# Performance work log

Measured on AMD Instinct MI355X. Metric: run time of the kernel, lower is better.

## Reference

```python
import jax, jax.numpy as jnp
import numpy as np

A, B, S, AD, H, NH = 8, 32768, 128, 16, 64, 4
D = H // NH  # attend_dim = 16
MAX_ACTION = 1.0


def setup_inputs() -> dict:
    key = jax.random.key(0)
    ks = jax.random.split(key, 16)
    sc = 0.05
    return {
        'states': jax.random.normal(ks[0], (A, B, S), jnp.float32),
        'actions': jax.random.normal(ks[1], (A, B, AD), jnp.float32),
        'Ws': jax.random.normal(ks[2], (S, H), jnp.float32) * sc,
        'bs': jnp.zeros((H,), jnp.float32),
        'We': jax.random.normal(ks[3], (S + AD, H), jnp.float32) * sc,
        'be': jnp.zeros((H,), jnp.float32),
        'Wk': jax.random.normal(ks[4], (NH, H, D), jnp.float32) * sc,
        'Wsel': jax.random.normal(ks[5], (NH, H, D), jnp.float32) * sc,
        'Wv': jax.random.normal(ks[6], (NH, H, D), jnp.float32) * sc,
        'bv': jnp.zeros((NH, D), jnp.float32),
        'W1': jax.random.normal(ks[7], (2 * H, H), jnp.float32) * sc,
        'b1': jnp.zeros((H,), jnp.float32),
        'W2': jax.random.normal(ks[8], (H, 1), jnp.float32) * sc,
        'b2': jnp.zeros((1,), jnp.float32),
    }


def reference(states, actions, Ws, bs, We, be, Wk, Wsel, Wv, bv, W1, b1, W2, b2):
    # per-agent encoders (shared params, as in the torch module)
    s_enc = jax.nn.relu(jnp.einsum('abs,sh->abh', states, Ws) + bs)          # [A,B,H]
    sa = jnp.concatenate([states, actions / MAX_ACTION], axis=-1)            # [A,B,S+AD]
    sa_enc = jax.nn.relu(jnp.einsum('abi,ih->abh', sa, We) + be)             # [A,B,H]

    # per-head keys / values / selectors (n = head axis)
    keys = jnp.einsum('abh,nhd->nabd', sa_enc, Wk)                           # [NH,A,B,D]
    vals = jax.nn.relu(jnp.einsum('abh,nhd->nabd', sa_enc, Wv) + bv[:, None, None, :])
    sel = jnp.einsum('abh,nhd->nabd', s_enc, Wsel)                           # [NH,A,B,D]

    # exclude-self attention over agents == masked softmax over agent axis j
    logits = jnp.einsum('nibd,njbd->nibj', sel, keys) / jnp.sqrt(jnp.float32(D))
    self_mask = jnp.eye(A, dtype=bool)                                       # [A(i),A(j)]
    logits = jnp.where(self_mask[None, :, None, :], -1e9, logits)
    w = jax.nn.softmax(logits, axis=-1)                                      # [NH,A,B,A]
    other = jnp.einsum('nibj,njbd->nibd', w, vals)                           # [NH,A,B,D]
    other_cat = jnp.transpose(other, (1, 2, 0, 3)).reshape(A, B, NH * D)     # [A,B,H]

    critic_in = jnp.concatenate([sa_enc, other_cat], axis=-1)                # [A,B,2H]
    h = jax.nn.relu(jnp.einsum('abi,ih->abh', critic_in, W1) + b1)
    q = jnp.einsum('abh,ho->abo', h, W2) + b2                                # [A,B,1]
    return q
```

## Files before the change

### kernel.cpp

```cpp
#include <hip/hip_runtime.h>
#include <hip/hip_bf16.h>

#define A_N 8
#define B_N 32768
#define S_N 128
#define AD_N 16

typedef __attribute__((ext_vector_type(8))) short short8;
typedef __attribute__((ext_vector_type(4))) float floatx4;
typedef __attribute__((ext_vector_type(4))) int intx4;

#define MFMA16(a, b, c) __builtin_amdgcn_mfma_f32_16x16x32_bf16(a, b, c, 0, 0, 0)
#define SBAR() __builtin_amdgcn_sched_barrier(0)

__device__ __forceinline__ short f2bf(float f) {
    __hip_bfloat16 h = __float2bfloat16(f);
    return *reinterpret_cast<short*>(&h);
}
__device__ __forceinline__ int pk(float a, float b) {
    __hip_bfloat162 p = __float22bfloat162_rn(make_float2(a, b));
    return *reinterpret_cast<int*>(&p);
}
__device__ __forceinline__ short8 mk8(int a, int b, int c, int d) {
    intx4 v = {a, b, c, d};
    return *reinterpret_cast<short8*>(&v);
}
__device__ __forceinline__ void pk2(short8& r, int i, float a, float b) {
    __hip_bfloat162 p = __float22bfloat162_rn(make_float2(a, b));
    short2 s = *reinterpret_cast<short2*>(&p);
    r[i] = s.x; r[i + 1] = s.y;
}
__device__ __forceinline__ short8 cvt8(float4 x0, float4 x1) {
    short8 r;
    pk2(r, 0, x0.x, x0.y); pk2(r, 2, x0.z, x0.w);
    pk2(r, 4, x1.x, x1.y); pk2(r, 6, x1.z, x1.w);
    return r;
}

__device__ __forceinline__ int chperm(int p) {
    return 32 * (p >> 5) + 16 * ((p & 7) >> 2) + 4 * ((p >> 3) & 3) + (p & 3);
}

#define OFF_Ws   10240
#define OFF_Wk   18432
#define OFF_Wsel 22528
#define OFF_Wv   26624
#define OFF_W1   30720
#define W_TOTAL  38912

__global__ void prep_weights(const float* __restrict__ Ws, const float* __restrict__ We,
                             const float* __restrict__ be,
                             const float* __restrict__ Wk, const float* __restrict__ Wsel,
                             const float* __restrict__ Wv, const float* __restrict__ W1,
                             short* __restrict__ w) {
    int idx = blockIdx.x * 256 + threadIdx.x;
    if (idx >= W_TOTAL) return;
    float v = 0.f;
    int i, base;
    if (idx < OFF_Ws)        { i = idx;            base = 0; }
    else if (idx < OFF_Wk)   { i = idx - OFF_Ws;   base = 1; }
    else if (idx < OFF_Wsel) { i = idx - OFF_Wk;   base = 2; }
    else if (idx < OFF_Wv)   { i = idx - OFF_Wsel; base = 3; }
    else if (idx < OFF_W1)   { i = idx - OFF_Wv;   base = 4; }
    else                     { i = idx - OFF_W1;   base = 5; }
    const int e   = i & 7;
    const int f   = i >> 3;
    const int ch  = f & 63;
    const int slq = f >> 6;
    const int p   = (slq >> 2) * 32 + (slq & 3) * 8 + e;
    if (base == 0)      v = (p < 144) ? We[p * 64 + ch] : (p == 144 ? be[ch] : 0.f);
    else if (base == 1) v = Ws[p * 64 + ch];
    else if (base == 2) v = Wk[(ch >> 4) * 1024 + chperm(p) * 16 + (ch & 15)];
    else if (base == 3) v = Wsel[(ch >> 4) * 1024 + chperm(p) * 16 + (ch & 15)];
    else if (base == 4) v = Wv[(ch >> 4) * 1024 + chperm(p) * 16 + (ch & 15)];
    else                v = W1[chperm(p) * 64 + ch];
    w[idx] = f2bf(v);
}

#define PAIRS 4

__global__ __launch_bounds__(512, 2)
void attention_critic_mfma(
    const float* __restrict__ states, const float* __restrict__ actions,
    const float* __restrict__ bs, const float* __restrict__ bv,
    const float* __restrict__ b1, const float* __restrict__ W2,
    const float* __restrict__ b2,
    const short* __restrict__ wts, float* __restrict__ out)
{
    __shared__ __align__(16) short smem[W_TOTAL];

    const int tid  = threadIdx.x;
    const int wv   = tid >> 6;
    const int lane = tid & 63;
    const int lq   = lane >> 4;
    const int ln   = lane & 15;

    for (int c = wv; c < 76; c += 8) {
        const unsigned int* g = reinterpret_cast<const unsigned int*>(wts + c * 512) + lane * 4;
        __builtin_amdgcn_global_load_lds(g, reinterpret_cast<unsigned int*>(smem + c * 512), 16, 0, 0);
    }

    const int lo = lq * 512 + ln * 8;
    const short* lbA = smem + lo;
    const short* lbB = smem + OFF_Wv + lo;

    float bS4[4], bv4[4], b14[4], w24[4];
    #pragma unroll
    for (int nt = 0; nt < 4; ++nt) {
        bS4[nt] = bs[nt * 16 + ln];
        bv4[nt] = bv[nt * 16 + ln];
        b14[nt] = b1[nt * 16 + ln];
        w24[nt] = W2[nt * 16 + ln];
    }
    const float b2v = b2[0];

    const int bbase = blockIdx.x * (PAIRS * 32);
    const int aA  = ln & 7;
    const int blA = ln >> 3;
    const float* srow = states  + ((long)aA * B_N + bbase + wv * 2 + blA) * S_N;
    const float* arow = actions + ((long)aA * B_N + bbase + wv * 2 + blA) * AD_N;

    __syncthreads();

    const floatx4 z = {0.f, 0.f, 0.f, 0.f};

    #pragma unroll 1
    for (int t = 0; t < PAIRS; ++t) {
        const int b0 = bbase + t * 32;

        short8 xf0[5], xf1[5];
        #pragma unroll
        for (int s = 0; s < 4; ++s) {
            float4 a0 = *reinterpret_cast<const float4*>(srow + s * 32 + lq * 8);
            float4 a1 = *reinterpret_cast<const float4*>(srow + s * 32 + lq * 8 + 4);
            float4 c0 = *reinterpret_cast<const float4*>(srow + 16 * S_N + s * 32 + lq * 8);
            float4 c1 = *reinterpret_cast<const float4*>(srow + 16 * S_N + s * 32 + lq * 8 + 4);
            xf0[s] = cvt8(a0, a1);
            xf1[s] = cvt8(c0, c1);
        }
        {
            short8 t0 = {0, 0, 0, 0, 0, 0, 0, 0}, t1 = t0;
            if (lq < 2) {
                float4 a0 = *reinterpret_cast<const float4*>(arow + lq * 8);
                float4 a1 = *reinterpret_cast<const float4*>(arow + lq * 8 + 4);
                float4 c0 = *reinterpret_cast<const float4*>(arow + 16 * AD_N + lq * 8);
                float4 c1 = *reinterpret_cast<const float4*>(arow + 16 * AD_N + lq * 8 + 4);
                t0 = cvt8(a0, a1);
                t1 = cvt8(c0, c1);
            } else if (lq == 2) {
                t0[0] = (short)0x3F80;
                t1[0] = (short)0x3F80;
            }
            xf0[4] = t0; xf1[4] = t1;
        }
        srow += 32 * S_N; arow += 32 * AD_N;

        short8 fE0[2], fE1[2];
        {
            floatx4 acc0[4] = {z, z, z, z}, acc1[4] = {z, z, z, z};
            #pragma unroll
            for (int s = 0; s < 5; ++s)
                #pragma unroll
                for (int nt = 0; nt < 4; ++nt) {
                    short8 wf = *reinterpret_cast<const short8*>(lbA + s * 2048 + nt * 128);
                    acc0[nt] = MFMA16(wf, xf0[s], acc0[nt]);
                    acc1[nt] = MFMA16(wf, xf1[s], acc1[nt]);
                }
            int p0[4][2], p1[4][2];
            #pragma unroll
            for (int nt = 0; nt < 4; ++nt) {
                p0[nt][0] = pk(fmaxf(acc0[nt][0], 0.f), fmaxf(acc0[nt][1], 0.f));
                p0[nt][1] = pk(fmaxf(acc0[nt][2], 0.f), fmaxf(acc0[nt][3], 0.f));
                p1[nt][0] = pk(fmaxf(acc1[nt][0], 0.f), fmaxf(acc1[nt][1], 0.f));
                p1[nt][1] = pk(fmaxf(acc1[nt][2], 0.f), fmaxf(acc1[nt][3], 0.f));
            }
            fE0[0] = mk8(p0[0][0], p0[0][1], p0[1][0], p0[1][1]);
            fE0[1] = mk8(p0[2][0], p0[2][1], p0[3][0], p0[3][1]);
            fE1[0] = mk8(p1[0][0], p1[0][1], p1[1][0], p1[1][1]);
            fE1[1] = mk8(p1[2][0], p1[2][1], p1[3][0], p1[3][1]);
        }
        SBAR();

        short8 fS0[2], fS1[2];
        {
            floatx4 acc0[4] = {z, z, z, z}, acc1[4] = {z, z, z, z};
            #pragma unroll
            for (int s = 0; s < 4; ++s)
                #pragma unroll
                for (int nt = 0; nt < 4; ++nt) {
                    short8 wf = *reinterpret_cast<const short8*>(lbA + OFF_Ws + s * 2048 + nt * 128);
                    acc0[nt] = MFMA16(wf, xf0[s], acc0[nt]);
                    acc1[nt] = MFMA16(wf, xf1[s], acc1[nt]);
                }
            int p0[4][2], p1[4][2];
            #pragma unroll
            for (int nt = 0; nt < 4; ++nt) {
                p0[nt][0] = pk(fmaxf(acc0[nt][0] + bS4[nt], 0.f), fmaxf(acc0[nt][1] + bS4[nt], 0.f));
                p0[nt][1] = pk(fmaxf(acc0[nt][2] + bS4[nt], 0.f), fmaxf(acc0[nt][3] + bS4[nt], 0.f));
                p1[nt][0] = pk(fmaxf(acc1[nt][0] + bS4[nt], 0.f), fmaxf(acc1[nt][1] + bS4[nt], 0.f));
                p1[nt][1] = pk(fmaxf(acc1[nt][2] + bS4[nt], 0.f), fmaxf(acc1[nt][3] + bS4[nt], 0.f));
            }
            fS0[0] = mk8(p0[0][0], p0[0][1], p0[1][0], p0[1][1]);
            fS0[1] = mk8(p0[2][0], p0[2][1], p0[3][0], p0[3][1]);
            fS1[0] = mk8(p1[0][0], p1[0][1], p1[1][0], p1[1][1]);
            fS1[1] = mk8(p1[2][0], p1[2][1], p1[3][0], p1[3][1]);
        }
        SBAR();

        int kp0[4][2], sp0[4][2], kp1[4][2], sp1[4][2];
        {
            floatx4 aK0[4] = {z, z, z, z}, aS0[4] = {z, z, z, z};
            floatx4 aK1[4] = {z, z, z, z}, aS1[4] = {z, z, z, z};
            #pragma unroll
            for (int s = 0; s < 2; ++s)
                #pragma unroll
                for (int nt = 0; nt < 4; ++nt) {
                    short8 wk = *reinterpret_cast<const short8*>(lbA + OFF_Wk   + s * 2048 + nt * 128);
                    short8 ws = *reinterpret_cast<const short8*>(lbA + OFF_Wsel + s * 2048 + nt * 128);
                    aK0[nt] = MFMA16(wk, fE0[s], aK0[nt]);
                    aK1[nt] = MFMA16(wk, fE1[s], aK1[nt]);
                    aS0[nt] = MFMA16(ws, fS0[s], aS0[nt]);
                    aS1[nt] = MFMA16(ws, fS1[s], aS1[nt]);
                }
            #pragma unroll
            for (int nt = 0; nt < 4; ++nt) {
                kp0[nt][0] = pk(aK0[nt][0], aK0[nt][1]); kp0[nt][1] = pk(aK0[nt][2], aK0[nt][3]);
                sp0[nt][0] = pk(aS0[nt][0], aS0[nt][1]); sp0[nt][1] = pk(aS0[nt][2], aS0[nt][3]);
                kp1[nt][0] = pk(aK1[nt][0], aK1[nt][1]); kp1[nt][1] = pk(aK1[nt][2], aK1[nt][3]);
                sp1[nt][0] = pk(aS1[nt][0], aS1[nt][1]); sp1[nt][1] = pk(aS1[nt][2], aS1[nt][3]);
            }
        }
        SBAR();

        int pV0[4][2], pV1[4][2];
        {
            floatx4 a0[4] = {z, z, z, z}, a1[4] = {z, z, z, z};
            #pragma unroll
            for (int s = 0; s < 2; ++s)
                #pragma unroll
                for (int nt = 0; nt < 4; ++nt) {
                    short8 wf = *reinterpret_cast<const short8*>(lbB + s * 2048 + nt * 128);
                    a0[nt] = MFMA16(fE0[s], wf, a0[nt]);
                    a1[nt] = MFMA16(fE1[s], wf, a1[nt]);
                }
            #pragma unroll
            for (int nt = 0; nt < 4; ++nt) {
                pV0[nt][0] = pk(fmaxf(a0[nt][0] + bv4[nt], 0.f), fmaxf(a0[nt][1] + bv4[nt], 0.f));
                pV0[nt][1] = pk(fmaxf(a0[nt][2] + bv4[nt], 0.f), fmaxf(a0[nt][3] + bv4[nt], 0.f));
                pV1[nt][0] = pk(fmaxf(a1[nt][0] + bv4[nt], 0.f), fmaxf(a1[nt][1] + bv4[nt], 0.f));
                pV1[nt][1] = pk(fmaxf(a1[nt][2] + bv4[nt], 0.f), fmaxf(a1[nt][3] + bv4[nt], 0.f));
            }
        }
        SBAR();

        int pO0[4][2], pO1[4][2];
        {
            const bool sameb = ((lq >> 1) == (ln >> 3));
            #pragma unroll
            for (int tt = 0; tt < 2; ++tt) {
                int (*kp)[2] = tt ? kp1 : kp0;
                int (*sp)[2] = tt ? sp1 : sp0;
                int (*pV)[2] = tt ? pV1 : pV0;
                int (*pO)[2] = tt ? pO1 : pO0;
                #pragma unroll
                for (int nt = 0; nt < 4; ++nt) {
                    short8 fa = mk8(kp[nt][0], kp[nt][1], 0, 0);
                    short8 fb = mk8(sp[nt][0], sp[nt][1], 0, 0);
                    floatx4 L = MFMA16(fa, fb, z);
                    float lg[4];
                    #pragma unroll
                    for (int i = 0; i < 4; ++i) {
                        const bool valid = sameb && (4 * lq + i != ln);
                        lg[i] = valid ? L[i] * 0.25f : -1e9f;
                    }
                    float m = fmaxf(fmaxf(lg[0], lg[1]), fmaxf(lg[2], lg[3]));
                    m = fmaxf(m, __shfl_xor(m, 16, 64));
                    m = fmaxf(m, __shfl_xor(m, 32, 64));
                    float e0 = __expf(lg[0] - m), e1 = __expf(lg[1] - m);
                    float e2 = __expf(lg[2] - m), e3 = __expf(lg[3] - m);
                    float ss = e0 + e1 + e2 + e3;
                    ss += __shfl_xor(ss, 16, 64);
                    ss += __shfl_xor(ss, 32, 64);
                    const float inv = 1.f / ss;
                    short8 fp = mk8(pk(e0 * inv, e1 * inv), pk(e2 * inv, e3 * inv), 0, 0);
                    short8 fv = mk8(pV[nt][0], pV[nt][1], 0, 0);
                    floatx4 O = MFMA16(fv, fp, z);
                    pO[nt][0] = pk(O[0], O[1]);
                    pO[nt][1] = pk(O[2], O[3]);
                }
            }
        }
        SBAR();

        {
            short8 fO0[2] = { mk8(pO0[0][0], pO0[0][1], pO0[1][0], pO0[1][1]),
                              mk8(pO0[2][0], pO0[2][1], pO0[3][0], pO0[3][1]) };
            short8 fO1[2] = { mk8(pO1[0][0], pO1[0][1], pO1[1][0], pO1[1][1]),
                              mk8(pO1[2][0], pO1[2][1], pO1[3][0], pO1[3][1]) };
            floatx4 aH0[4] = {z, z, z, z}, aH1[4] = {z, z, z, z};
            #pragma unroll
            for (int s = 0; s < 4; ++s) {
                const short8 a0 = (s < 2) ? fE0[s] : fO0[s - 2];
                const short8 a1 = (s < 2) ? fE1[s] : fO1[s - 2];
                #pragma unroll
                for (int nt = 0; nt < 4; ++nt) {
                    short8 w1 = *reinterpret_cast<const short8*>(lbB + 4096 + s * 2048 + nt * 128);
                    aH0[nt] = MFMA16(a0, w1, aH0[nt]);
                    aH1[nt] = MFMA16(a1, w1, aH1[nt]);
                }
            }
            #pragma unroll
            for (int tt = 0; tt < 2; ++tt) {
                floatx4* aH = tt ? aH1 : aH0;
                float p0 = 0.f, p1 = 0.f, p2 = 0.f, p3 = 0.f;
                #pragma unroll
                for (int nt = 0; nt < 4; ++nt) {
                    p0 += fmaxf(aH[nt][0] + b14[nt], 0.f) * w24[nt];
                    p1 += fmaxf(aH[nt][1] + b14[nt], 0.f) * w24[nt];
                    p2 += fmaxf(aH[nt][2] + b14[nt], 0.f) * w24[nt];
                    p3 += fmaxf(aH[nt][3] + b14[nt], 0.f) * w24[nt];
                }
                #pragma unroll
                for (int mk = 1; mk < 16; mk <<= 1) {
                    p0 += __shfl_xor(p0, mk, 64);
                    p1 += __shfl_xor(p1, mk, 64);
                    p2 += __shfl_xor(p2, mk, 64);
                    p3 += __shfl_xor(p3, mk, 64);
                }
                if (ln == 0) {
                    float pr[4] = {p0, p1, p2, p3};
                    const int bt = b0 + tt * 16;
                    #pragma unroll
                    for (int i = 0; i < 4; ++i) {
                        const int slot = lq * 4 + i;
                        out[(long)(slot & 7) * B_N + bt + wv * 2 + (slot >> 3)] = pr[i] + b2v;
                    }
                }
            }
        }
        SBAR();
    }
}

extern "C" void kernel_launch(void* const* d_in, const int* in_sizes, int n_in,
                              void* d_out, int out_size, void* d_ws, size_t ws_size,
                              hipStream_t stream) {
    const float* states  = (const float*)d_in[0];
    const float* actions = (const float*)d_in[1];
    const float* Ws      = (const float*)d_in[2];
    const float* bs      = (const float*)d_in[3];
    const float* We      = (const float*)d_in[4];
    const float* be      = (const float*)d_in[5];
    const float* Wk      = (const float*)d_in[6];
    const float* Wsel    = (const float*)d_in[7];
    const float* Wv      = (const float*)d_in[8];
    const float* bv      = (const float*)d_in[9];
    const float* W1      = (const float*)d_in[10];
    const float* b1      = (const float*)d_in[11];
    const float* W2      = (const float*)d_in[12];
    const float* b2      = (const float*)d_in[13];
    short* wts = (short*)d_ws;
    float* out = (float*)d_out;

    prep_weights<<<(W_TOTAL + 255) / 256, 256, 0, stream>>>(Ws, We, be, Wk, Wsel, Wv, W1, wts);
    attention_critic_mfma<<<B_N / (PAIRS * 32), 512, 0, stream>>>(
        states, actions, bs, bv, b1, W2, b2, wts, out);
}
```

Baseline: 234.9 us.

## Stage states/actions tiles into LDS asynchronously with swizzle and prefetch

Replaces direct per-thread global float4 loads of states and actions with global_load_lds staging into a per-wave swizzled LDS buffer. The next half-tile is prefetched while the current one runs its encoder MFMAs, so global latency is hidden behind compute. Phase-1 encoding is split into two sequential half-tile passes instead of interleaved dual accumulators. The cost is about 74KB of extra LDS per block and explicit waitcnt barriers, which may reduce occupancy (2 blocks of 512 threads) and cut MFMA interleaving.

Result: no change. 238.0 us (+1.3%).

```diff
diff --git a/kernel.cpp b/kernel.cpp
--- a/kernel.cpp
+++ b/kernel.cpp
@@ -35,6 +35,12 @@
     pk2(r, 0, x0.x, x0.y); pk2(r, 2, x0.z, x0.w);
     pk2(r, 4, x1.x, x1.y); pk2(r, 6, x1.z, x1.w);
     return r;
+}
+__device__ __forceinline__ void wait_lgkm() {
+    asm volatile("s_waitcnt lgkmcnt(0)" ::: "memory");
+}
+__device__ __forceinline__ void wait_vm() {
+    asm volatile("s_waitcnt vmcnt(0)" ::: "memory");
 }
 
 __device__ __forceinline__ int chperm(int p) {
@@ -79,6 +85,94 @@
 
 #define PAIRS 4
 
+#define XB_WAVE 9216
+
+__device__ __forceinline__ void stage_tile(const float* __restrict__ states,
+                                           const float* __restrict__ actions,
+                                           char* xb, int btw, int lane) {
+    const int bl  = lane >> 5;
+    const int c16 = (lane & 31) << 4;
+    #pragma unroll
+    for (int a = 0; a < 8; ++a) {
+        const int r = 2 * a + bl;
+        const char* src = (const char*)states
+            + (((long)(a * B_N + btw + bl)) << 9)
+            + (c16 ^ ((r & 7) << 4));
+        __builtin_amdgcn_global_load_lds((const unsigned int*)src,
+            (unsigned int*)(xb + a * 1024), 16, 0, 0);
+    }
+    {
+        const int ra  = lane >> 2;
+        const char* src = (const char*)actions
+            + (((long)((lane >> 3) * B_N + btw + ((lane >> 2) & 1))) << 6)
+            + (((lane & 3) << 4) ^ ((ra & 6) << 3));
+        __builtin_amdgcn_global_load_lds((const unsigned int*)src,
+            (unsigned int*)(xb + 8192), 16, 0, 0);
+    }
+}
+
+__device__ __forceinline__ void load_xf(const char* xb, int r, int lq, short8* xf) {
+    const int ss = (r & 7) << 4;
+    const char* rb = xb + (r << 9);
+    #pragma unroll
+    for (int s = 0; s < 4; ++s) {
+        const int c = (s << 7) + (lq << 5);
+        float4 f0 = *reinterpret_cast<const float4*>(rb + ((c)      ^ ss));
+        float4 f1 = *reinterpret_cast<const float4*>(rb + ((c + 16) ^ ss));
+        xf[s] = cvt8(f0, f1);
+    }
+    short8 xt = {0, 0, 0, 0, 0, 0, 0, 0};
+    if (lq < 2) {
+        const int as = (r & 6) << 3;
+        const char* ab = xb + 8192 + (r << 6);
+        const int c = lq << 5;
+        float4 f0 = *reinterpret_cast<const float4*>(ab + ((c)      ^ as));
+        float4 f1 = *reinterpret_cast<const float4*>(ab + ((c + 16) ^ as));
+        xt = cvt8(f0, f1);
+    } else if (lq == 2) {
+        xt[0] = (short)0x3F80;
+    }
+    xf[4] = xt;
+}
+
+__device__ __forceinline__ void do_phase1(const short8* xf, const short* lbA,
+                                          const float* bS4, short8* fE, short8* fS) {
+    const floatx4 z = {0.f, 0.f, 0.f, 0.f};
+    {
+        floatx4 acc[4] = {z, z, z, z};
+        #pragma unroll
+        for (int s = 0; s < 5; ++s)
+            #pragma unroll
+            for (int nt = 0; nt < 4; ++nt)
+                acc[nt] = MFMA16(*reinterpret_cast<const short8*>(lbA + s * 2048 + nt * 128), xf[s], acc[nt]);
+        int p[4][2];
+        #pragma unroll
+        for (int nt = 0; nt < 4; ++nt) {
+            p[nt][0] = pk(fmaxf(acc[nt][0], 0.f), fmaxf(acc[nt][1], 0.f));
+            p[nt][1] = pk(fmaxf(acc[nt][2], 0.f), fmaxf(acc[nt][3], 0.f));
+        }
+        fE[0] = mk8(p[0][0], p[0][1], p[1][0], p[1][1]);
+        fE[1] = mk8(p[2][0], p[2][1], p[3][0], p[3][1]);
+    }
+    SBAR();
+    {
+        floatx4 acc[4] = {z, z, z, z};
+        #pragma unroll
+        for (int s = 0; s < 4; ++s)
+            #pragma unroll
+            for (int nt = 0; nt < 4; ++nt)
+                acc[nt] = MFMA16(*reinterpret_cast<const short8*>(lbA + OFF_Ws + s * 2048 + nt * 128), xf[s], acc[nt]);
+        int p[4][2];
+        #pragma unroll
+        for (int nt = 0; nt < 4; ++nt) {
+            p[nt][0] = pk(fmaxf(acc[nt][0] + bS4[nt], 0.f), fmaxf(acc[nt][1] + bS4[nt], 0.f));
+            p[nt][1] = pk(fmaxf(acc[nt][2] + bS4[nt], 0.f), fmaxf(acc[nt][3] + bS4[nt], 0.f));
+        }
+        fS[0] = mk8(p[0][0], p[0][1], p[1][0], p[1][1]);
+        fS[1] = mk8(p[2][0], p[2][1], p[3][0], p[3][1]);
+    }
+}
+
 __global__ __launch_bounds__(512, 2)
 void attention_critic_mfma(
     const float* __restrict__ states, const float* __restrict__ actions,
@@ -87,7 +181,7 @@
     const float* __restrict__ b2,
     const short* __restrict__ wts, float* __restrict__ out)
 {
-    __shared__ __align__(16) short smem[W_TOTAL];
+    __shared__ __align__(16) short smem[W_TOTAL + 8 * (XB_WAVE / 2)];
 
     const int tid  = threadIdx.x;
     const int wv   = tid >> 6;
@@ -103,6 +197,8 @@
     const int lo = lq * 512 + ln * 8;
     const short* lbA = smem + lo;
     const short* lbB = smem + OFF_Wv + lo;
+
+    char* xb = reinterpret_cast<char*>(smem + W_TOTAL) + wv * XB_WAVE;
 
     float bS4[4], bv4[4], b14[4], w24[4];
     #pragma unroll
@@ -115,96 +211,35 @@
     const float b2v = b2[0];
 
     const int bbase = blockIdx.x * (PAIRS * 32);
-    const int aA  = ln & 7;
-    const int blA = ln >> 3;
-    const float* srow = states  + ((long)aA * B_N + bbase + wv * 2 + blA) * S_N;
-    const float* arow = actions + ((long)aA * B_N + bbase + wv * 2 + blA) * AD_N;
-
+    const int rX = ((ln & 7) << 1) | (ln >> 3);
+
+    stage_tile(states, actions, xb, bbase + wv * 2, lane);
     __syncthreads();
 
     const floatx4 z = {0.f, 0.f, 0.f, 0.f};
 
     #pragma unroll 1
     for (int t = 0; t < PAIRS; ++t) {
-        const int b0 = bbase + t * 32;
-
-        short8 xf0[5], xf1[5];
-        #pragma unroll
-        for (int s = 0; s < 4; ++s) {
-            float4 a0 = *reinterpret_cast<const float4*>(srow + s * 32 + lq * 8);
-            float4 a1 = *reinterpret_cast<const float4*>(srow + s * 32 + lq * 8 + 4);
-            float4 c0 = *reinterpret_cast<const float4*>(srow + 16 * S_N + s * 32 + lq * 8);
-            float4 c1 = *reinterpret_cast<const float4*>(srow + 16 * S_N + s * 32 + lq * 8 + 4);
-            xf0[s] = cvt8(a0, a1);
-            xf1[s] = cvt8(c0, c1);
-        }
-        {
-            short8 t0 = {0, 0, 0, 0, 0, 0, 0, 0}, t1 = t0;
-            if (lq < 2) {
-                float4 a0 = *reinterpret_cast<const float4*>(arow + lq * 8);
-                float4 a1 = *reinterpret_cast<const float4*>(arow + lq * 8 + 4);
-                float4 c0 = *reinterpret_cast<const float4*>(arow + 16 * AD_N + lq * 8);
-                float4 c1 = *reinterpret_cast<const float4*>(arow + 16 * AD_N + lq * 8 + 4);
-                t0 = cvt8(a0, a1);
-                t1 = cvt8(c0, c1);
-            } else if (lq == 2) {
-                t0[0] = (short)0x3F80;
-                t1[0] = (short)0x3F80;
-            }
-            xf0[4] = t0; xf1[4] = t1;
-        }
-        srow += 32 * S_N; arow += 32 * AD_N;
-
-        short8 fE0[2], fE1[2];
-        {
-            floatx4 acc0[4] = {z, z, z, z}, acc1[4] = {z, z, z, z};
-            #pragma unroll
-            for (int s = 0; s < 5; ++s)
-                #pragma unroll
-                for (int nt = 0; nt < 4; ++nt) {
-                    short8 wf = *reinterpret_cast<const short8*>(lbA + s * 2048 + nt * 128);
-                    acc0[nt] = MFMA16(wf, xf0[s], acc0[nt]);
-                    acc1[nt] = MFMA16(wf, xf1[s], acc1[nt]);
-                }
-            int p0[4][2], p1[4][2];
-            #pragma unroll
-            for (int nt = 0; nt < 4; ++nt) {
-                p0[nt][0] = pk(fmaxf(acc0[nt][0], 0.f), fmaxf(acc0[nt][1], 0.f));
-                p0[nt][1] = pk(fmaxf(acc0[nt][2], 0.f), fmaxf(acc0[nt][3], 0.f));
-                p1[nt][0] = pk(fmaxf(acc1[nt][0], 0.f), fmaxf(acc1[nt][1], 0.f));
-                p1[nt][1] = pk(fmaxf(acc1[nt][2], 0.f), fmaxf(acc1[nt][3], 0.f));
-            }
-            fE0[0] = mk8(p0[0][0], p0[0][1], p0[1][0], p0[1][1]);
-            fE0[1] = mk8(p0[2][0], p0[2][1], p0[3][0], p0[3][1]);
-            fE1[0] = mk8(p1[0][0], p1[0][1], p1[1][0], p1[1][1]);
-            fE1[1] = mk8(p1[2][0], p1[2][1], p1[3][0], p1[3][1]);
-        }
-        SBAR();
-
-        short8 fS0[2], fS1[2];
-        {
-            floatx4 acc0[4] = {z, z, z, z}, acc1[4] = {z, z, z, z};
-            #pragma unroll
-            for (int s = 0; s < 4; ++s)
-                #pragma unroll
-                for (int nt = 0; nt < 4; ++nt) {
-                    short8 wf = *reinterpret_cast<const short8*>(lbA + OFF_Ws + s * 2048 + nt * 128);
-                    acc0[nt] = MFMA16(wf, xf0[s], acc0[nt]);
-                    acc1[nt] = MFMA16(wf, xf1[s], acc1[nt]);
-                }
-            int p0[4][2], p1[4][2];
-            #pragma unroll
-            for (int nt = 0; nt < 4; ++nt) {
-                p0[nt][0] = pk(fmaxf(acc0[nt][0] + bS4[nt], 0.f), fmaxf(acc0[nt][1] + bS4[nt], 0.f));
-                p0[nt][1] = pk(fmaxf(acc0[nt][2] + bS4[nt], 0.f), fmaxf(acc0[nt][3] + bS4[nt], 0.f));
-                p1[nt][0] = pk(fmaxf(acc1[nt][0] + bS4[nt], 0.f), fmaxf(acc1[nt][1] + bS4[nt], 0.f));
-                p1[nt][1] = pk(fmaxf(acc1[nt][2] + bS4[nt], 0.f), fmaxf(acc1[nt][3] + bS4[nt], 0.f));
-            }
-            fS0[0] = mk8(p0[0][0], p0[0][1], p0[1][0], p0[1][1]);
-            fS0[1] = mk8(p0[2][0], p0[2][1], p0[3][0], p0[3][1]);
-            fS1[0] = mk8(p1[0][0], p1[0][1], p1[1][0], p1[1][1]);
-            fS1[1] = mk8(p1[2][0], p1[2][1], p1[3][0], p1[3][1]);
-        }
+        const int b0   = bbase + t * 32;
+        const int btw0 = b0 + wv * 2;
+
+        short8 xf0[5];
+        wait_vm(); SBAR();
+        load_xf(xb, rX, lq, xf0);
+        wait_lgkm(); SBAR();
+        stage_tile(states, actions, xb, btw0 + 16, lane);
+        short8 fE0[2], fS0[2];
+        do_phase1(xf0, lbA, bS4, fE0, fS0);
+        SBAR();
+
+        short8 xf1[5];
+        wait_vm(); SBAR();
+        load_xf(xb, rX, lq, xf1);
+        wait_lgkm(); SBAR();
+        if (t + 1 < PAIRS)
+            stage_tile(states, actions, xb, btw0 + 32, lane);
+        short8 fE1[2], fS1[2];
+        do_phase1(xf1, lbA, bS4, fE1, fS1);
         SBAR();
 
         int kp0[4][2], sp0[4][2], kp1[4][2], sp1[4][2];
```
